# Kernel tuning notes

Measured on AMD Instinct MI355X. Metric: run time of the kernel, lower is better.

The kernel has to match this reference:

```python
import jax, jax.numpy as jnp
import numpy as np

B, N, D, D_MODEL = 4, 2048, 512, 512


def setup_inputs() -> dict:
    key = jax.random.key(0)
    kx, kq, kk, kv, ks = jax.random.split(key, 5)
    scale = 1.0 / np.sqrt(D)
    x = jax.random.normal(kx, (B, N, D), dtype=jnp.float32)
    Wq = (jax.random.normal(kq, (D, D_MODEL), dtype=jnp.float32) * scale)
    Wk = (jax.random.normal(kk, (D, D_MODEL), dtype=jnp.float32) * scale)
    Wv = (jax.random.normal(kv, (D, D_MODEL), dtype=jnp.float32) * scale)
    Ws = (jax.random.normal(ks, (D, 1), dtype=jnp.float32) * scale)
    return {"x": x, "Wq": Wq, "Wk": Wk, "Wv": Wv, "Ws": Ws}


def reference(x, Wq, Wk, Wv, Ws):
    # Projections (Linear, no bias)
    Q = x @ Wq                      # (B, N, d_model)
    K = x @ Wk                      # (B, N, d_model)
    V = x @ Wv                      # (B, N, d_model)
    sigma = x @ Ws                  # (B, N, 1)

    n = x.shape[1]
    dm = Wq.shape[1]

    # Prior association: Gaussian kernel over |i-j| distance, row-normalized
    idx = jnp.arange(n)
    dist = jnp.abs(idx[:, None] - idx[None, :]).astype(x.dtype)      # (N, N)
    inv_norm = 1.0 / (jnp.sqrt(2.0 * jnp.pi).astype(x.dtype) * jnp.abs(sigma))
    gaussian = inv_norm * jnp.exp(-0.5 * jnp.square(dist[None] / sigma))  # (B,N,N)
    P = gaussian / jnp.sum(gaussian, axis=-1, keepdims=True)

    # Series association: scaled dot-product softmax attention
    scores = jnp.einsum('bnd,bmd->bnm', Q, K) / jnp.sqrt(jnp.asarray(dm, x.dtype))
    S = jax.nn.softmax(scores, axis=-1)                               # (B,N,N)

    # Reconstruction
    Z = S @ V                                                          # (B,N,d_model)
    return (Z, P)
```

## Files before the change

kernel.cpp:

```cpp
#include <hip/hip_runtime.h>

typedef float f32x4 __attribute__((ext_vector_type(4)));
typedef short s16x8 __attribute__((ext_vector_type(8)));
typedef unsigned short us4 __attribute__((ext_vector_type(4)));

#define MFMA16(a, b, c) __builtin_amdgcn_mfma_f32_16x16x32_bf16(a, b, c, 0, 0, 0)

#define GLOAD_LDS16(gp, lp) __builtin_amdgcn_global_load_lds( \
    (__attribute__((address_space(1))) void*)(gp),            \
    (__attribute__((address_space(3))) void*)(lp), 16, 0, 0)

__device__ __forceinline__ unsigned short f2bf(float f) {
    union { float f; unsigned u; } v; v.f = f;
    unsigned r = v.u + 0x7fffu + ((v.u >> 16) & 1u);
    return (unsigned short)(r >> 16);
}

__device__ __forceinline__ void gemm_core128(
    const unsigned short* __restrict__ Ab, size_t Astride,
    const unsigned short* __restrict__ Bb, size_t Bstride,
    int K, unsigned short* As, unsigned short* Bs,
    int t, f32x4 acc[4][4])
{
    const int wave = t >> 6, lane = t & 63;
    const int c = lane & 15, quad = lane >> 4;
    const int wm = (wave >> 1) * 64, wn = (wave & 1) * 64;
    const int srow = t >> 2;
    const int scol = (t & 3) * 8;

    for (int k0 = 0; k0 < K; k0 += 32) {
        __syncthreads();
        const unsigned short* ga = Ab + (size_t)srow * Astride + k0 + scol;
        const unsigned short* gb = Bb + (size_t)srow * Bstride + k0 + scol;
        GLOAD_LDS16(ga,                 As + t * 8);
        GLOAD_LDS16(ga + 64 * Astride,  As + 2048 + t * 8);
        GLOAD_LDS16(gb,                 Bs + t * 8);
        GLOAD_LDS16(gb + 64 * Bstride,  Bs + 2048 + t * 8);
        __syncthreads();

        s16x8 af[4], bf[4];
        #pragma unroll
        for (int i = 0; i < 4; i++)
            af[i] = *(const s16x8*)(As + (wm + i * 16 + c) * 32 + quad * 8);
        #pragma unroll
        for (int i = 0; i < 4; i++)
            bf[i] = *(const s16x8*)(Bs + (wn + i * 16 + c) * 32 + quad * 8);
        #pragma unroll
        for (int mt = 0; mt < 4; mt++)
            #pragma unroll
            for (int nt = 0; nt < 4; nt++)
                acc[mt][nt] = MFMA16(af[mt], bf[nt], acc[mt][nt]);
    }
}

__global__ __launch_bounds__(256) void k_convert(
    const float* __restrict__ x, const float* __restrict__ wq,
    const float* __restrict__ wk, const float* __restrict__ wv,
    unsigned short* __restrict__ xbf, unsigned short* __restrict__ wt,
    float* __restrict__ lg)
{
    int bid = blockIdx.x, t = threadIdx.x;
    if (bid < 4096) {
        int gid = bid * 256 + t;
        float4 v = ((const float4*)x)[gid];
        us4 o = { f2bf(v.x), f2bf(v.y), f2bf(v.z), f2bf(v.w) };
        ((us4*)xbf)[gid] = o;
    } else if (bid < 7168) {
        int idx = (bid - 4096) * 256 + t;
        int w = idx >> 18;
        int r = idx & 262143;
        int k = r >> 9, n = r & 511;
        const float* src = (w == 0) ? wq : (w == 1) ? wk : wv;
        wt[((size_t)(w * 512 + n) << 9) + k] = f2bf(src[r]);
    } else {
        lg[(bid - 7168) * 256 + t] = 0.f;
    }
}

__global__ __launch_bounds__(256) void k_proj(
    const unsigned short* __restrict__ xbf, const unsigned short* __restrict__ wt,
    unsigned short* __restrict__ qbf, unsigned short* __restrict__ kbf,
    unsigned short* __restrict__ vtbf)
{
    __shared__ __align__(16) unsigned short As[128 * 32];
    __shared__ __align__(16) unsigned short Bs[128 * 32];

    int t = threadIdx.x;
    int m0 = blockIdx.x * 128, n0 = blockIdx.y * 128;
    f32x4 acc[4][4] = {};

    gemm_core128(xbf + (size_t)m0 * 512, 512, wt + (size_t)n0 * 512, 512,
                 512, As, Bs, t, acc);

    int wave = t >> 6, lane = t & 63, c = lane & 15, quad = lane >> 4;
    int wm = (wave >> 1) * 64, wn = (wave & 1) * 64;
    int sel = blockIdx.y >> 2;

    if (sel < 2) {
        unsigned short* dst = sel ? kbf : qbf;
        int ncol0 = n0 - sel * 512;
        #pragma unroll
        for (int mt = 0; mt < 4; mt++) {
            #pragma unroll
            for (int nt = 0; nt < 4; nt++) {
                int col = ncol0 + wn + nt * 16 + c;
                #pragma unroll
                for (int r = 0; r < 4; r++) {
                    int rw = m0 + wm + mt * 16 + quad * 4 + r;
                    dst[(size_t)rw * 512 + col] = f2bf(acc[mt][nt][r]);
                }
            }
        }
    } else {
        #pragma unroll
        for (int mt = 0; mt < 4; mt++) {
            int rw0 = m0 + wm + mt * 16 + quad * 4;
            int bb = rw0 >> 11, nn = rw0 & 2047;
            #pragma unroll
            for (int nt = 0; nt < 4; nt++) {
                int d = (n0 - 1024) + wn + nt * 16 + c;
                us4 pk = { f2bf(acc[mt][nt][0]), f2bf(acc[mt][nt][1]),
                           f2bf(acc[mt][nt][2]), f2bf(acc[mt][nt][3]) };
                *(us4*)(vtbf + ((size_t)(bb * 512 + d)) * 2048 + nn) = pk;
            }
        }
    }
}

__device__ __forceinline__ void score_body(
    const unsigned short* __restrict__ qbf, const unsigned short* __restrict__ kbf,
    unsigned short* __restrict__ pbf, float* __restrict__ lg,
    int b, int m0, int n0, int t, unsigned short* As, unsigned short* Bs)
{
    f32x4 acc[4][4] = {};
    gemm_core128(qbf + (size_t)(b * 2048 + m0) * 512, 512,
                 kbf + (size_t)(b * 2048 + n0) * 512, 512,
                 512, As, Bs, t, acc);

    int wave = t >> 6, lane = t & 63, c = lane & 15, quad = lane >> 4;
    int wm = (wave >> 1) * 64, wn = (wave & 1) * 64;
    const float scale = 0.044194173824159216f;

    #pragma unroll
    for (int mt = 0; mt < 4; mt++) {
        #pragma unroll
        for (int r = 0; r < 4; r++) {
            int row = m0 + wm + mt * 16 + quad * 4 + r;
            float rs = 0.f;
            #pragma unroll
            for (int nt = 0; nt < 4; nt++) {
                float p = __expf(acc[mt][nt][r] * scale);
                rs += p;
                pbf[(size_t)(b * 2048 + row) * 2048 + n0 + wn + nt * 16 + c] = f2bf(p);
            }
            rs += __shfl_xor(rs, 1, 16);
            rs += __shfl_xor(rs, 2, 16);
            rs += __shfl_xor(rs, 4, 16);
            rs += __shfl_xor(rs, 8, 16);
            if (c == 0) atomicAdd(&lg[b * 2048 + row], rs);
        }
    }
}

__device__ __forceinline__ void prior_body(
    const float* __restrict__ x, const float* __restrict__ wsv,
    float* __restrict__ pout, int blk, int t, float* red, float* red2)
{
    int i = blk & 2047;
    const float* xr = x + (size_t)blk * 512;

    float part = xr[t] * wsv[t] + xr[t + 256] * wsv[t + 256];
    #pragma unroll
    for (int o = 32; o; o >>= 1) part += __shfl_xor(part, o, 64);
    if ((t & 63) == 0) red[t >> 6] = part;
    __syncthreads();
    float sigma = red[0] + red[1] + red[2] + red[3];

    float inv2 = 0.5f / (sigma * sigma);
    float g[8];
    float sum = 0.f;
    int j0 = t * 8;
    #pragma unroll
    for (int u = 0; u < 8; u++) {
        int j = j0 + u;
        float d = (float)(j - i);
        g[u] = (j == i) ? 1.0f : __expf(-(d * d) * inv2);
        sum += g[u];
    }
    #pragma unroll
    for (int o = 32; o; o >>= 1) sum += __shfl_xor(sum, o, 64);
    if ((t & 63) == 0) red2[t >> 6] = sum;
    __syncthreads();
    float inv = 1.0f / (red2[0] + red2[1] + red2[2] + red2[3]);

    float* pr = pout + (size_t)blk * 2048 + j0;
    float4 o0 = { g[0] * inv, g[1] * inv, g[2] * inv, g[3] * inv };
    float4 o1 = { g[4] * inv, g[5] * inv, g[6] * inv, g[7] * inv };
    ((float4*)pr)[0] = o0;
    ((float4*)pr)[1] = o1;
}

__global__ __launch_bounds__(256) void k_score_prior(
    const unsigned short* __restrict__ qbf, const unsigned short* __restrict__ kbf,
    unsigned short* __restrict__ pbf, float* __restrict__ lg,
    const float* __restrict__ x, const float* __restrict__ wsv,
    float* __restrict__ pout)
{
    __shared__ __align__(16) unsigned short As[128 * 32];
    __shared__ __align__(16) unsigned short Bs[128 * 32];
    __shared__ float red[4];
    __shared__ float red2[4];

    int bid = blockIdx.x, t = threadIdx.x;
    if (bid < 1024) {
        int b = bid >> 8, r = bid & 255;
        score_body(qbf, kbf, pbf, lg, b, (r & 15) * 128, (r >> 4) * 128, t, As, Bs);
    } else {
        prior_body(x, wsv, pout, bid - 1024, t, red, red2);
    }
}

__global__ __launch_bounds__(256) void k_score(
    const unsigned short* __restrict__ qbf, const unsigned short* __restrict__ kbf,
    unsigned short* __restrict__ pbf, float* __restrict__ lg)
{
    __shared__ __align__(16) unsigned short As[128 * 32];
    __shared__ __align__(16) unsigned short Bs[128 * 32];
    score_body(qbf, kbf, pbf, lg, blockIdx.z,
               blockIdx.x * 128, blockIdx.y * 128, threadIdx.x, As, Bs);
}

__global__ __launch_bounds__(256) void k_out(
    const unsigned short* __restrict__ pbf, const unsigned short* __restrict__ vtbf,
    const float* __restrict__ lg, float* __restrict__ zout)
{
    __shared__ __align__(16) unsigned short As[128 * 32];
    __shared__ __align__(16) unsigned short Bs[64 * 32];
    __shared__ float invl[128];

    int t = threadIdx.x;
    int b = blockIdx.z;
    int m0 = blockIdx.x * 128, n0 = blockIdx.y * 64;

    if (t < 128) invl[t] = 1.0f / lg[b * 2048 + m0 + t];

    const unsigned short* Ab = pbf + (size_t)(b * 2048 + m0) * 2048;
    const unsigned short* Bb = vtbf + (size_t)(b * 512 + n0) * 2048;

    const int wave = t >> 6, lane = t & 63;
    const int c = lane & 15, quad = lane >> 4;
    const int wm = (wave >> 1) * 64, wn = (wave & 1) * 32;
    const int srow = t >> 2;
    const int scol = (t & 3) * 8;

    f32x4 acc[4][2] = {};

    for (int k0 = 0; k0 < 2048; k0 += 32) {
        __syncthreads();
        const unsigned short* ga = Ab + (size_t)srow * 2048 + k0 + scol;
        GLOAD_LDS16(ga,             As + t * 8);
        GLOAD_LDS16(ga + 64 * 2048, As + 2048 + t * 8);
        GLOAD_LDS16(Bb + (size_t)srow * 2048 + k0 + scol, Bs + t * 8);
        __syncthreads();

        s16x8 af[4], bf[2];
        #pragma unroll
        for (int i = 0; i < 4; i++)
            af[i] = *(const s16x8*)(As + (wm + i * 16 + c) * 32 + quad * 8);
        #pragma unroll
        for (int i = 0; i < 2; i++)
            bf[i] = *(const s16x8*)(Bs + (wn + i * 16 + c) * 32 + quad * 8);
        #pragma unroll
        for (int mt = 0; mt < 4; mt++)
            #pragma unroll
            for (int nt = 0; nt < 2; nt++)
                acc[mt][nt] = MFMA16(af[mt], bf[nt], acc[mt][nt]);
    }

    #pragma unroll
    for (int mt = 0; mt < 4; mt++) {
        #pragma unroll
        for (int nt = 0; nt < 2; nt++) {
            #pragma unroll
            for (int r = 0; r < 4; r++) {
                int row = wm + mt * 16 + quad * 4 + r;
                zout[(size_t)(b * 2048 + m0 + row) * 512 + n0 + wn + nt * 16 + c]
                    = acc[mt][nt][r] * invl[row];
            }
        }
    }
}

__global__ __launch_bounds__(256) void k_prior(
    const float* __restrict__ x, const float* __restrict__ wsv,
    float* __restrict__ pout)
{
    __shared__ float red[4];
    __shared__ float red2[4];
    prior_body(x, wsv, pout, blockIdx.x, threadIdx.x, red, red2);
}

extern "C" void kernel_launch(void* const* d_in, const int* in_sizes, int n_in,
                              void* d_out, int out_size, void* d_ws, size_t ws_size,
                              hipStream_t stream)
{
    const float* x  = (const float*)d_in[0];
    const float* wq = (const float*)d_in[1];
    const float* wk = (const float*)d_in[2];
    const float* wv = (const float*)d_in[3];
    const float* ws = (const float*)d_in[4];

    float* zout = (float*)d_out;
    float* pout = zout + (size_t)4 * 2048 * 512;

    const size_t need = ((size_t)4194304 + 786432 + 3 * 4194304 + 16777216) * 2
                        + 8192 * 4;

    if (ws_size >= need) {
        unsigned short* base = (unsigned short*)d_ws;
        unsigned short* xbf  = base;
        unsigned short* wt   = xbf  + (size_t)4194304;
        unsigned short* qbf  = wt   + (size_t)786432;
        unsigned short* kbf  = qbf  + (size_t)4194304;
        unsigned short* vtbf = kbf  + (size_t)4194304;
        unsigned short* pbf  = vtbf + (size_t)4194304;
        float*          lg   = (float*)(pbf + (size_t)16777216);

        k_convert<<<dim3(7200), dim3(256), 0, stream>>>(x, wq, wk, wv, xbf, wt, lg);
        k_proj       <<<dim3(64, 12),   dim3(256), 0, stream>>>(xbf, wt, qbf, kbf, vtbf);
        k_score_prior<<<dim3(9216),     dim3(256), 0, stream>>>(qbf, kbf, pbf, lg, x, ws, pout);
        k_out        <<<dim3(16, 8, 4), dim3(256), 0, stream>>>(pbf, vtbf, lg, zout);
    } else {
        unsigned short* base = (unsigned short*)pout;
        unsigned short* pbf  = base;
        unsigned short* qbf  = base + (size_t)16777216;
        unsigned short* kbf  = qbf  + (size_t)4194304;
        unsigned short* vtbf = kbf  + (size_t)4194304;
        float*          lg   = (float*)(vtbf + (size_t)4194304);
        unsigned short* xbf  = base;
        unsigned short* wt   = base + (size_t)4194304;

        k_convert<<<dim3(7200), dim3(256), 0, stream>>>(x, wq, wk, wv, xbf, wt, lg);
        k_proj  <<<dim3(64, 12),    dim3(256), 0, stream>>>(xbf, wt, qbf, kbf, vtbf);
        k_score <<<dim3(16, 16, 4), dim3(256), 0, stream>>>(qbf, kbf, pbf, lg);
        k_out   <<<dim3(16, 8, 4),  dim3(256), 0, stream>>>(pbf, vtbf, lg, zout);
        k_prior <<<dim3(8192),      dim3(256), 0, stream>>>(x, ws, pout);
    }
}
```

Measured before the change: 208.1 us.

## Swap GEMM operand roles so epilogues write packed contiguous vectors

The Q/K projection, score and output GEMMs swap their A and B operands, so each lane's four accumulator values fall on contiguous output addresses. Epilogues then issue packed us4 or float4 stores instead of scattered 2-byte or 4-byte stores, which cuts the number of store instructions on the large P matrix and on Z. The row-sum reduction for the softmax denominator moves from a 16-lane shuffle tree to two cross-quad shuffles. Store coalescing across lanes changes in exchange, since adjacent lanes now write to different rows.

```diff
diff --git a/kernel.cpp b/kernel.cpp
--- a/kernel.cpp
+++ b/kernel.cpp
@@ -38,18 +38,18 @@
         GLOAD_LDS16(gb + 64 * Bstride,  Bs + 2048 + t * 8);
         __syncthreads();
 
-        s16x8 af[4], bf[4];
+        s16x8 af[4], bfr[4];
         #pragma unroll
         for (int i = 0; i < 4; i++)
             af[i] = *(const s16x8*)(As + (wm + i * 16 + c) * 32 + quad * 8);
         #pragma unroll
         for (int i = 0; i < 4; i++)
-            bf[i] = *(const s16x8*)(Bs + (wn + i * 16 + c) * 32 + quad * 8);
+            bfr[i] = *(const s16x8*)(Bs + (wn + i * 16 + c) * 32 + quad * 8);
         #pragma unroll
         for (int mt = 0; mt < 4; mt++)
             #pragma unroll
             for (int nt = 0; nt < 4; nt++)
-                acc[mt][nt] = MFMA16(af[mt], bf[nt], acc[mt][nt]);
+                acc[mt][nt] = MFMA16(af[mt], bfr[nt], acc[mt][nt]);
     }
 }
 
@@ -86,32 +86,35 @@
     __shared__ __align__(16) unsigned short Bs[128 * 32];
 
     int t = threadIdx.x;
-    int m0 = blockIdx.x * 128, n0 = blockIdx.y * 128;
-    f32x4 acc[4][4] = {};
-
-    gemm_core128(xbf + (size_t)m0 * 512, 512, wt + (size_t)n0 * 512, 512,
-                 512, As, Bs, t, acc);
-
     int wave = t >> 6, lane = t & 63, c = lane & 15, quad = lane >> 4;
     int wm = (wave >> 1) * 64, wn = (wave & 1) * 64;
-    int sel = blockIdx.y >> 2;
-
-    if (sel < 2) {
-        unsigned short* dst = sel ? kbf : qbf;
-        int ncol0 = n0 - sel * 512;
+    f32x4 acc[4][4] = {};
+
+    if (blockIdx.y < 8) {
+        int m0 = blockIdx.y * 128;
+        int tok0 = blockIdx.x * 128;
+        gemm_core128(wt + (size_t)m0 * 512, 512, xbf + (size_t)tok0 * 512, 512,
+                     512, As, Bs, t, acc);
+
+        unsigned short* dst = (m0 < 512) ? qbf : kbf;
+        int mbase = m0 & 511;
         #pragma unroll
         for (int mt = 0; mt < 4; mt++) {
+            int dim0 = mbase + wm + mt * 16 + quad * 4;
             #pragma unroll
             for (int nt = 0; nt < 4; nt++) {
-                int col = ncol0 + wn + nt * 16 + c;
-                #pragma unroll
-                for (int r = 0; r < 4; r++) {
-                    int rw = m0 + wm + mt * 16 + quad * 4 + r;
-                    dst[(size_t)rw * 512 + col] = f2bf(acc[mt][nt][r]);
-                }
+                int token = tok0 + wn + nt * 16 + c;
+                us4 pk = { f2bf(acc[mt][nt][0]), f2bf(acc[mt][nt][1]),
+                           f2bf(acc[mt][nt][2]), f2bf(acc[mt][nt][3]) };
+                *(us4*)(dst + (size_t)token * 512 + dim0) = pk;
             }
         }
     } else {
+        int m0 = blockIdx.x * 128;
+        int n0 = 1024 + (blockIdx.y - 8) * 128;
+        gemm_core128(xbf + (size_t)m0 * 512, 512, wt + (size_t)n0 * 512, 512,
+                     512, As, Bs, t, acc);
+
         #pragma unroll
         for (int mt = 0; mt < 4; mt++) {
             int rw0 = m0 + wm + mt * 16 + quad * 4;
@@ -130,11 +133,11 @@
 __device__ __forceinline__ void score_body(
     const unsigned short* __restrict__ qbf, const unsigned short* __restrict__ kbf,
     unsigned short* __restrict__ pbf, float* __restrict__ lg,
-    int b, int m0, int n0, int t, unsigned short* As, unsigned short* Bs)
+    int b, int kt0, int q0, int t, unsigned short* As, unsigned short* Bs)
 {
     f32x4 acc[4][4] = {};
-    gemm_core128(qbf + (size_t)(b * 2048 + m0) * 512, 512,
-                 kbf + (size_t)(b * 2048 + n0) * 512, 512,
+    gemm_core128(kbf + (size_t)(b * 2048 + kt0) * 512, 512,
+                 qbf + (size_t)(b * 2048 + q0) * 512, 512,
                  512, As, Bs, t, acc);
 
     int wave = t >> 6, lane = t & 63, c = lane & 15, quad = lane >> 4;
@@ -142,23 +145,24 @@
     const float scale = 0.044194173824159216f;
 
     #pragma unroll
-    for (int mt = 0; mt < 4; mt++) {
-        #pragma unroll
-        for (int r = 0; r < 4; r++) {
-            int row = m0 + wm + mt * 16 + quad * 4 + r;
-            float rs = 0.f;
-            #pragma unroll
-            for (int nt = 0; nt < 4; nt++) {
+    for (int nt = 0; nt < 4; nt++) {
+        int q = q0 + wn + nt * 16 + c;
+        float rs = 0.f;
+        unsigned short* pr = pbf + (size_t)(b * 2048 + q) * 2048 + kt0 + wm + quad * 4;
+        #pragma unroll
+        for (int mt = 0; mt < 4; mt++) {
+            us4 pk;
+            #pragma unroll
+            for (int r = 0; r < 4; r++) {
                 float p = __expf(acc[mt][nt][r] * scale);
                 rs += p;
-                pbf[(size_t)(b * 2048 + row) * 2048 + n0 + wn + nt * 16 + c] = f2bf(p);
+                pk[r] = f2bf(p);
             }
-            rs += __shfl_xor(rs, 1, 16);
-            rs += __shfl_xor(rs, 2, 16);
-            rs += __shfl_xor(rs, 4, 16);
-            rs += __shfl_xor(rs, 8, 16);
-            if (c == 0) atomicAdd(&lg[b * 2048 + row], rs);
+            *(us4*)(pr + mt * 16) = pk;
         }
+        rs += __shfl_xor(rs, 16);
+        rs += __shfl_xor(rs, 32);
+        if (quad == 0) atomicAdd(&lg[b * 2048 + q], rs);
     }
 }
 
@@ -234,59 +238,59 @@
     const unsigned short* __restrict__ pbf, const unsigned short* __restrict__ vtbf,
     const float* __restrict__ lg, float* __restrict__ zout)
 {
-    __shared__ __align__(16) unsigned short As[128 * 32];
-    __shared__ __align__(16) unsigned short Bs[64 * 32];
+    __shared__ __align__(16) unsigned short As[64 * 32];
+    __shared__ __align__(16) unsigned short Bs[128 * 32];
     __shared__ float invl[128];
 
     int t = threadIdx.x;
     int b = blockIdx.z;
-    int m0 = blockIdx.x * 128, n0 = blockIdx.y * 64;
-
-    if (t < 128) invl[t] = 1.0f / lg[b * 2048 + m0 + t];
-
-    const unsigned short* Ab = pbf + (size_t)(b * 2048 + m0) * 2048;
-    const unsigned short* Bb = vtbf + (size_t)(b * 512 + n0) * 2048;
+    int d0 = blockIdx.x * 64, q0 = blockIdx.y * 128;
+
+    if (t < 128) invl[t] = 1.0f / lg[b * 2048 + q0 + t];
+
+    const unsigned short* Ab = vtbf + (size_t)(b * 512 + d0) * 2048;
+    const unsigned short* Bb = pbf + (size_t)(b * 2048 + q0) * 2048;
 
     const int wave = t >> 6, lane = t & 63;
     const int c = lane & 15, quad = lane >> 4;
-    const int wm = (wave >> 1) * 64, wn = (wave & 1) * 32;
+    const int wm = (wave >> 1) * 32, wn = (wave & 1) * 64;
     const int srow = t >> 2;
     const int scol = (t & 3) * 8;
 
-    f32x4 acc[4][2] = {};
+    f32x4 acc[2][4] = {};
 
     for (int k0 = 0; k0 < 2048; k0 += 32) {
         __syncthreads();
-        const unsigned short* ga = Ab + (size_t)srow * 2048 + k0 + scol;
-        GLOAD_LDS16(ga,             As + t * 8);
-        GLOAD_LDS16(ga + 64 * 2048, As + 2048 + t * 8);
-        GLOAD_LDS16(Bb + (size_t)srow * 2048 + k0 + scol, Bs + t * 8);
+        GLOAD_LDS16(Ab + (size_t)srow * 2048 + k0 + scol, As + t * 8);
+        const unsigned short* gb = Bb + (size_t)srow * 2048 + k0 + scol;
+        GLOAD_LDS16(gb,             Bs + t * 8);
+        GLOAD_LDS16(gb + 64 * 2048, Bs + 2048 + t * 8);
         __syncthreads();
 
-        s16x8 af[4], bf[2];
+        s16x8 af[2], bfr[4];
+        #pragma unroll
+        for (int i = 0; i < 2; i++)
+            af[i] = *(const s16x8*)(As + (wm + i * 16 + c) * 32 + quad * 8);
         #pragma unroll
         for (int i = 0; i < 4; i++)
-            af[i] = *(const s16x8*)(As + (wm + i * 16 + c) * 32 + quad * 8);
-        #pragma unroll
-        for (int i = 0; i < 2; i++)
-            bf[i] = *(const s16x8*)(Bs + (wn + i * 16 + c) * 32 + quad * 8);
-        #pragma unroll
-        for (int mt = 0; mt < 4; mt++)
-            #pragma unroll
-            for (int nt = 0; nt < 2; nt++)
-                acc[mt][nt] = MFMA16(af[mt], bf[nt], acc[mt][nt]);
-    }
-
-    #pragma unroll
-    for (int mt = 0; mt < 4; mt++) {
-        #pragma unroll
-        for (int nt = 0; nt < 2; nt++) {
-            #pragma unroll
-            for (int r = 0; r < 4; r++) {
-                int row = wm + mt * 16 + quad * 4 + r;
-                zout[(size_t)(b * 2048 + m0 + row) * 512 + n0 + wn + nt * 16 + c]
-                    = acc[mt][nt][r] * invl[row];
-            }
+            bfr[i] = *(const s16x8*)(Bs + (wn + i * 16 + c) * 32 + quad * 8);
+        #pragma unroll
+        for (int mt = 0; mt < 2; mt++)
+            #pragma unroll
+            for (int nt = 0; nt < 4; nt++)
+                acc[mt][nt] = MFMA16(af[mt], bfr[nt], acc[mt][nt]);
+    }
+
+    #pragma unroll
+    for (int mt = 0; mt < 2; mt++) {
+        int dd = wm + mt * 16 + quad * 4;
+        #pragma unroll
+        for (int nt = 0; nt < 4; nt++) {
+            int qi = wn + nt * 16 + c;
+            float il = invl[qi];
+            float4 o = { acc[mt][nt][0] * il, acc[mt][nt][1] * il,
+                         acc[mt][nt][2] * il, acc[mt][nt][3] * il };
+            *(float4*)(zout + (size_t)(b * 2048 + q0 + qi) * 512 + d0 + dd) = o;
         }
     }
 }
@@ -329,7 +333,7 @@
         k_convert<<<dim3(7200), dim3(256), 0, stream>>>(x, wq, wk, wv, xbf, wt, lg);
         k_proj       <<<dim3(64, 12),   dim3(256), 0, stream>>>(xbf, wt, qbf, kbf, vtbf);
         k_score_prior<<<dim3(9216),     dim3(256), 0, stream>>>(qbf, kbf, pbf, lg, x, ws, pout);
-        k_out        <<<dim3(16, 8, 4), dim3(256), 0, stream>>>(pbf, vtbf, lg, zout);
+        k_out        <<<dim3(8, 16, 4), dim3(256), 0, stream>>>(pbf, vtbf, lg, zout);
     } else {
         unsigned short* base = (unsigned short*)pout;
         unsigned short* pbf  = base;
@@ -343,7 +347,7 @@
         k_convert<<<dim3(7200), dim3(256), 0, stream>>>(x, wq, wk, wv, xbf, wt, lg);
         k_proj  <<<dim3(64, 12),    dim3(256), 0, stream>>>(xbf, wt, qbf, kbf, vtbf);
         k_score <<<dim3(16, 16, 4), dim3(256), 0, stream>>>(qbf, kbf, pbf, lg);
-        k_out   <<<dim3(16, 8, 4),  dim3(256), 0, stream>>>(pbf, vtbf, lg, zout);
+        k_out   <<<dim3(8, 16, 4),  dim3(256), 0, stream>>>(pbf, vtbf, lg, zout);
         k_prior <<<dim3(8192),      dim3(256), 0, stream>>>(x, ws, pout);
     }
 }
```

Result: slower. 215.1 us (+3.4%).
